# Kernel optimization log

Measured on AMD Instinct MI355X. Metric: run time of the kernel, lower is better.

The kernel has to match this reference:

```python
import jax, jax.numpy as jnp
import numpy as np

HID = 1024; INTER = 2048; NSTATE = 16; KCONV = 4; DTRANK = 64
NHEADS = 16; NKV = 4; HDIM = 64; VHDIM = 128; EPS = 1e-6
ATTN_H = HID; K_H = NKV * HDIM; V_H = NKV * VHDIM
LATENT = INTER + ATTN_H + K_H + V_H  # 3840


def rmsnorm(x, w, eps=EPS):
    return x * jax.lax.rsqrt(jnp.mean(x * x, axis=-1, keepdims=True) + eps) * w


def setup_inputs():
    key = jax.random.key(0)
    ks = jax.random.split(key, 8)
    B, S = 2, 2048
    s = 0.02
    x = jax.random.normal(ks[0], (B, S, HID), jnp.float32)
    W_in = jax.random.normal(ks[1], (LATENT + INTER, HID), jnp.float32) * s
    conv_w = jax.random.normal(ks[2], (INTER, KCONV), jnp.float32) * 0.2
    conv_b = jnp.zeros((INTER,), jnp.float32)
    W_x = jax.random.normal(ks[3], (DTRANK + 2 * NSTATE, INTER), jnp.float32) * s
    dt_ln_w = jnp.ones((DTRANK,), jnp.float32)
    B_ln_w = jnp.ones((NSTATE,), jnp.float32)
    C_ln_w = jnp.ones((NSTATE,), jnp.float32)
    W_dt = jax.random.normal(ks[4], (INTER, DTRANK), jnp.float32) * s
    b_dt = jnp.log(jnp.expm1(jnp.full((INTER,), 0.01, jnp.float32)))
    A_log = jnp.log(jnp.broadcast_to(jnp.arange(1, NSTATE + 1, dtype=jnp.float32)[None, :], (INTER, NSTATE)))
    D_param = jnp.ones((INTER,), jnp.float32)
    ln1_w = jnp.ones((INTER,), jnp.float32)
    ln2_w = jnp.ones((INTER,), jnp.float32)
    W_out = jax.random.normal(ks[5], (HID, INTER), jnp.float32) * s
    return {"x": x, "W_in": W_in, "conv_w": conv_w, "conv_b": conv_b, "W_x": W_x,
            "dt_ln_w": dt_ln_w, "B_ln_w": B_ln_w, "C_ln_w": C_ln_w, "W_dt": W_dt,
            "b_dt": b_dt, "A_log": A_log, "D_param": D_param, "ln1_w": ln1_w,
            "ln2_w": ln2_w, "W_out": W_out}


def reference(x, W_in, conv_w, conv_b, W_x, dt_ln_w, B_ln_w, C_ln_w, W_dt, b_dt,
              A_log, D_param, ln1_w, ln2_w, W_out):
    Bsz, S, _ = x.shape
    proj = x @ W_in.T  # [B,S,LATENT+INTER]
    q = proj[..., :ATTN_H]
    k = proj[..., ATTN_H:ATTN_H + K_H]
    v = proj[..., ATTN_H + K_H:ATTN_H + K_H + V_H]
    xs = proj[..., ATTN_H + K_H + V_H:LATENT]
    gate = proj[..., LATENT:]

    # depthwise causal conv1d + silu (causal_conv1d_fn)
    xt = xs.transpose(0, 2, 1)  # [B,D,S]
    xc = jax.lax.conv_general_dilated(xt, conv_w[:, None, :], (1,), [(KCONV - 1, 0)],
                                      feature_group_count=INTER,
                                      dimension_numbers=("NCH", "OIH", "NCH"))
    xc = jax.nn.silu(xc + conv_b[None, :, None]).transpose(0, 2, 1)  # [B,S,D]

    # input-dependent dt, B, C with inner RMSNorms
    ssm_p = xc @ W_x.T  # [B,S,DTRANK+2N]
    dt = rmsnorm(ssm_p[..., :DTRANK], dt_ln_w)
    Bm = rmsnorm(ssm_p[..., DTRANK:DTRANK + NSTATE], B_ln_w)
    Cm = rmsnorm(ssm_p[..., DTRANK + NSTATE:], C_ln_w)
    delta = jax.nn.softplus(dt @ W_dt.T + b_dt)  # [B,S,D] (delta_bias + softplus)
    A = -jnp.exp(A_log)  # [D,N]

    def step(h, inp):
        d_t, b_t, c_t, x_t = inp  # [B,D],[B,N],[B,N],[B,D]
        dA = jnp.exp(d_t[:, :, None] * A)  # [B,D,N]
        h = h * dA + (d_t * x_t)[:, :, None] * b_t[:, None, :]
        y = jnp.einsum("bdn,bn->bd", h, c_t)
        return h, y

    h0 = jnp.zeros((Bsz, INTER, NSTATE), x.dtype)
    _, ys = jax.lax.scan(step, h0, (delta.transpose(1, 0, 2), Bm.transpose(1, 0, 2),
                                    Cm.transpose(1, 0, 2), xc.transpose(1, 0, 2)))
    y = ys.transpose(1, 0, 2) + xc * D_param
    y = y * jax.nn.silu(gate)  # gated scan output [B,S,INTER]

    # causal GQA attention branch (no output proj; v_head_dim = INTER/NHEADS)
    qh = q.reshape(Bsz, S, NHEADS, HDIM).transpose(0, 2, 1, 3)
    kh = jnp.repeat(k.reshape(Bsz, S, NKV, HDIM), NHEADS // NKV, axis=2).transpose(0, 2, 1, 3)
    vh = jnp.repeat(v.reshape(Bsz, S, NKV, VHDIM), NHEADS // NKV, axis=2).transpose(0, 2, 1, 3)
    scores = jnp.einsum("bhqd,bhkd->bhqk", qh, kh) * (1.0 / float(np.sqrt(HDIM)))
    mask = jnp.tril(jnp.ones((S, S), bool))
    scores = jnp.where(mask, scores, jnp.finfo(scores.dtype).min)
    attn = jnp.einsum("bhqk,bhkd->bhqd", jax.nn.softmax(scores, axis=-1), vh)
    attn = attn.transpose(0, 2, 1, 3).reshape(Bsz, S, INTER)

    out = (rmsnorm(attn, ln1_w) + rmsnorm(y, ln2_w)) * 0.5
    return out @ W_out.T
```

## Files before the change

### kernel.cpp

```cpp
#include <hip/hip_runtime.h>
#include <stdint.h>

#define HID    1024
#define INTER  2048
#define NSTATE 16
#define DTRANK 64
#define NHEADS 16
#define NKV    4
#define HDIM   64
#define VHDIM  128
#define ATTN_H 1024
#define K_H    256
#define V_H    512
#define LATENT 3840
#define NCOLS  5888
#define BATCH  2
#define SEQ    2048
#define T_TOT  4096
#define NCHUNK 64
#define CHLEN  32
#define LOG2E  1.44269504f

typedef __bf16 bf16x8 __attribute__((ext_vector_type(8)));
typedef float  f32x4  __attribute__((ext_vector_type(4)));
typedef float  f32x4v __attribute__((ext_vector_type(4)));
typedef unsigned short u16x8 __attribute__((ext_vector_type(8)));

__device__ __forceinline__ float bf2f(unsigned short u) {
    return __uint_as_float(((unsigned int)u) << 16);
}
__device__ __forceinline__ unsigned short f2bf(float f) {
    unsigned int u = __float_as_uint(f);
    u = (u + 0x7fffu + ((u >> 16) & 1u)) >> 16;
    return (unsigned short)u;
}
__device__ __forceinline__ bf16x8 ldb8(const unsigned short* p) {
    return __builtin_bit_cast(bf16x8, *(const u16x8*)p);
}

typedef const __attribute__((address_space(1))) unsigned int* gas_ptr;
typedef __attribute__((address_space(3))) unsigned int* las_ptr;
__device__ __forceinline__ void load_lds16(const void* g, void* l) {
    __builtin_amdgcn_global_load_lds((gas_ptr)g, (las_ptr)l, 16, 0, 0);
}

__global__ void k_prep(const float* __restrict__ x, const float* __restrict__ W_in,
                       const float* __restrict__ W_dt, const float* __restrict__ W_out,
                       const float* __restrict__ W_x,
                       unsigned short* __restrict__ xbf, unsigned short* __restrict__ Winbf,
                       unsigned short* __restrict__ Wdtbf, unsigned short* __restrict__ Woutbf,
                       unsigned short* __restrict__ Wxpad) {
    int i = blockIdx.x * 256 + threadIdx.x;
    const float* src; unsigned short* dst; int off;
    if (i < 524288)        { src = x;     dst = xbf;    off = i; }
    else if (i < 1277952)  { src = W_in;  dst = Winbf;  off = i - 524288; }
    else if (i < 1294336)  { src = W_dt;  dst = Wdtbf;  off = i - 1277952; }
    else if (i < 1556480)  { src = W_out; dst = Woutbf; off = i - 1294336; }
    else {
        int e = (i - 1556480) * 8;
        int row = e >> 11, col = e & 2047;
        u16x8 o;
        if (row < DTRANK + 2 * NSTATE) {
#pragma unroll
            for (int k = 0; k < 8; k++) o[k] = f2bf(W_x[(size_t)row * INTER + col + k]);
        } else {
#pragma unroll
            for (int k = 0; k < 8; k++) o[k] = 0;
        }
        *(u16x8*)(Wxpad + e) = o;
        return;
    }
    f32x4v a = ((const f32x4v*)src)[2 * off];
    f32x4v b = ((const f32x4v*)src)[2 * off + 1];
    u16x8 o;
#pragma unroll
    for (int k = 0; k < 4; k++) { o[k] = f2bf(a[k]); o[k + 4] = f2bf(b[k]); }
    *(u16x8*)(dst + (size_t)off * 8) = o;
}

template <int NT>
__launch_bounds__(512)
__global__ void k_gemm8(const unsigned short* __restrict__ A, const unsigned short* __restrict__ B,
                        unsigned short* __restrict__ C, int lda, int ldb, int ldc) {
    __shared__ __align__(16) unsigned short As[3][256 * 64];
    __shared__ __align__(16) unsigned short Bs[3][128 * 64];
    const int tid = threadIdx.x;
    const int lane = tid & 63;
    const int w = tid >> 6;
    const int wm = w >> 1, wn = w & 1;
    const int l15 = lane & 15, hi = lane >> 4;
    const int nwg = gridDim.x * gridDim.y;
    int lin = blockIdx.y * gridDim.x + blockIdx.x;
    lin = (lin & 7) * (nwg >> 3) + (lin >> 3);
    const int bm = (lin / gridDim.x) * 256;
    const int bn = (lin % gridDim.x) * 128;

    const int srcCol = ((lane & 7) ^ (lane >> 3)) * 8;

    auto stageA = [&](int buf, int kt, int u) {
        int rsb = 64 * u + 8 * w;
        load_lds16(A + (size_t)(bm + rsb + (lane >> 3)) * lda + kt * 64 + srcCol, &As[buf][rsb * 64]);
    };
    auto stageB = [&](int buf, int kt, int u) {
        int rsb = 64 * u + 8 * w;
        load_lds16(B + (size_t)(bn + rsb + (lane >> 3)) * ldb + kt * 64 + srcCol, &Bs[buf][rsb * 64]);
    };

    f32x4 acc[4][4];
#pragma unroll
    for (int i = 0; i < 4; i++)
#pragma unroll
        for (int j = 0; j < 4; j++) acc[i][j] = (f32x4){0.f, 0.f, 0.f, 0.f};

    auto phase = [&](int buf, int kk, auto stageThunk, int vm) {
        bf16x8 a_[4], b_[4];
        const int cc = (kk << 2) + hi;
#pragma unroll
        for (int mi = 0; mi < 4; ++mi) {
            int row = 64 * wm + 16 * mi + l15;
            a_[mi] = ldb8(&As[buf][row * 64 + ((cc ^ (row & 7)) << 3)]);
        }
#pragma unroll
        for (int ni = 0; ni < 4; ++ni) {
            int row = 64 * wn + 16 * ni + l15;
            b_[ni] = ldb8(&Bs[buf][row * 64 + ((cc ^ (row & 7)) << 3)]);
        }
        stageThunk();
        if (vm == 1)      asm volatile("s_waitcnt vmcnt(6)" ::: "memory");
        else if (vm == 2) asm volatile("s_waitcnt vmcnt(0)" ::: "memory");
        __builtin_amdgcn_s_barrier();
        __builtin_amdgcn_s_setprio(1);
#pragma unroll
        for (int mi = 0; mi < 4; ++mi)
#pragma unroll
            for (int ni = 0; ni < 4; ++ni)
                acc[mi][ni] = __builtin_amdgcn_mfma_f32_16x16x32_bf16(a_[mi], b_[ni], acc[mi][ni], 0, 0, 0);
        __builtin_amdgcn_s_setprio(0);
        __builtin_amdgcn_s_barrier();
    };

#pragma unroll
    for (int u = 0; u < 4; ++u) stageA(0, 0, u);
    stageB(0, 0, 0); stageB(0, 0, 1);
#pragma unroll
    for (int u = 0; u < 4; ++u) stageA(1, 1, u);
    stageB(1, 1, 0); stageB(1, 1, 1);
    asm volatile("s_waitcnt vmcnt(6)" ::: "memory");
    __builtin_amdgcn_s_barrier();

    int buf = 0;
    for (int t = 0; t < NT; ++t) {
        const int kt = t + 2;
        const bool st = kt < NT;
        const int pbuf = (buf + 2 >= 3) ? buf - 1 : buf + 2;
        phase(buf, 0, [&] {
            if (st) { stageA(pbuf, kt, 0); stageA(pbuf, kt, 1); stageA(pbuf, kt, 2); }
        }, 0);
        phase(buf, 1, [&] {
            if (st) { stageA(pbuf, kt, 3); stageB(pbuf, kt, 0); stageB(pbuf, kt, 1); }
        }, st ? 1 : 2);
        buf = (buf + 1 >= 3) ? 0 : buf + 1;
    }

#pragma unroll
    for (int mi = 0; mi < 4; ++mi)
#pragma unroll
        for (int ni = 0; ni < 4; ++ni)
#pragma unroll
            for (int r = 0; r < 4; ++r) {
                int grow = bm + 64 * wm + 16 * mi + (hi << 2) + r;
                int gcol = bn + 64 * wn + 16 * ni + l15;
                C[(size_t)grow * ldc + gcol] = f2bf(acc[mi][ni][r]);
            }
}

template <int OUT_MODE>
__launch_bounds__(256)
__global__ void k_gemm(const unsigned short* __restrict__ A, const unsigned short* __restrict__ B,
                       void* __restrict__ Cout, const float* __restrict__ bias,
                       int M, int N, int K, int lda, int ldb, int ldc) {
    __shared__ __align__(16) unsigned short As[128 * 64];
    __shared__ __align__(16) unsigned short Bs[128 * 64];
    const int tid = threadIdx.x;
    const int lane = tid & 63;
    const int w = tid >> 6;
    const int wm = w >> 1, wn = w & 1;
    const int nwg = gridDim.x * gridDim.y;
    int lin = blockIdx.y * gridDim.x + blockIdx.x;
    lin = (lin & 7) * (nwg >> 3) + (lin >> 3);
    const int bm = (lin / gridDim.x) * 128, bn = (lin % gridDim.x) * 128;
    const size_t koff = (OUT_MODE == 3) ? (size_t)blockIdx.z * K : 0;

    f32x4 acc[4][4];
#pragma unroll
    for (int i = 0; i < 4; i++)
#pragma unroll
        for (int j = 0; j < 4; j++) acc[i][j] = (f32x4){0.f, 0.f, 0.f, 0.f};

    const int nk = K >> 6;
    for (int ks = 0; ks < nk; ++ks) {
        const int k0 = ks << 6;
#pragma unroll
        for (int i = 0; i < 4; ++i) {
            int qb = (w << 6) + (i << 8);
            int q = qb + lane;
            int row = q >> 3, c = q & 7;
            int csrc = c ^ (row & 7);
            load_lds16(A + (size_t)(bm + row) * lda + koff + k0 + csrc * 8, As + qb * 8);
            load_lds16(B + (size_t)(bn + row) * ldb + koff + k0 + csrc * 8, Bs + qb * 8);
        }
        __syncthreads();
#pragma unroll
        for (int kk = 0; kk < 2; ++kk) {
            bf16x8 af[4], bfr[4];
#pragma unroll
            for (int mi = 0; mi < 4; mi++) {
                int row = (wm << 6) + (mi << 4) + (lane & 15);
                int c = (kk << 2) + (lane >> 4);
                af[mi] = ldb8(As + row * 64 + (c ^ (row & 7)) * 8);
            }
#pragma unroll
            for (int ni = 0; ni < 4; ni++) {
                int row = (wn << 6) + (ni << 4) + (lane & 15);
                int c = (kk << 2) + (lane >> 4);
                bfr[ni] = ldb8(Bs + row * 64 + (c ^ (row & 7)) * 8);
            }
#pragma unroll
            for (int mi = 0; mi < 4; mi++)
#pragma unroll
                for (int ni = 0; ni < 4; ni++)
                    acc[mi][ni] = __builtin_amdgcn_mfma_f32_16x16x32_bf16(af[mi], bfr[ni], acc[mi][ni], 0, 0, 0);
        }
        __syncthreads();
    }
#pragma unroll
    for (int mi = 0; mi < 4; mi++)
#pragma unroll
        for (int ni = 0; ni < 4; ni++)
#pragma unroll
            for (int r = 0; r < 4; r++) {
                int grow = bm + (wm << 6) + (mi << 4) + ((lane >> 4) << 2) + r;
                int gcol = bn + (wn << 6) + (ni << 4) + (lane & 15);
                float v = acc[mi][ni][r];
                if (OUT_MODE == 0) {
                    ((unsigned short*)Cout)[(size_t)grow * ldc + gcol] = f2bf(v);
                } else if (OUT_MODE == 1) {
                    ((float*)Cout)[(size_t)grow * ldc + gcol] = v;
                } else if (OUT_MODE == 3) {
                    ((float*)Cout)[(size_t)blockIdx.z * M * ldc + (size_t)grow * ldc + gcol] = v;
                } else {
                    v += bias[gcol];
                    v = (v > 20.f) ? v : log1pf(__expf(v));
                    ((unsigned short*)Cout)[(size_t)grow * ldc + gcol] = f2bf(v);
                }
            }
}

__global__ void k_conv(const unsigned short* __restrict__ proj, const float* __restrict__ conv_w,
                       const float* __restrict__ conv_b, unsigned short* __restrict__ xc) {
    int r = blockIdx.x;
    int d8 = threadIdx.x * 8;
    int t = r & (SEQ - 1);
    float accv[8];
#pragma unroll
    for (int i = 0; i < 8; i++) accv[i] = conv_b[d8 + i];
#pragma unroll
    for (int j = 0; j < 4; j++) {
        int tp = t - 3 + j;
        if (tp < 0) continue;
        u16x8 xv = *(const u16x8*)(proj + (size_t)(r - 3 + j) * NCOLS + (LATENT - INTER) + d8);
#pragma unroll
        for (int i = 0; i < 8; i++) accv[i] += conv_w[(d8 + i) * 4 + j] * bf2f(xv[i]);
    }
    u16x8 o;
#pragma unroll
    for (int i = 0; i < 8; i++) {
        float v = accv[i];
        v = v / (1.f + __expf(-v));
        o[i] = f2bf(v);
    }
    *(u16x8*)(xc + (size_t)r * INTER + d8) = o;
}

__global__ void k_rms3(const float* __restrict__ ssmp, const float* __restrict__ dt_w,
                       const float* __restrict__ B_w, const float* __restrict__ C_w,
                       unsigned short* __restrict__ dtbf, float* __restrict__ Bm, float* __restrict__ Cm) {
    int r = blockIdx.x;
    int tid = threadIdx.x;
    int lane = tid & 63, w = tid >> 6;
    int c = tid;
    float v = 0.f;
    if (c < 96) {
#pragma unroll
        for (int s = 0; s < 8; s++) v += ssmp[(size_t)s * (T_TOT * 128) + (size_t)r * 128 + c];
    }
    float s = v * v;
    if (w == 0) {
#pragma unroll
        for (int d = 1; d < 64; d <<= 1) s += __shfl_xor(s, d);
        float rms = rsqrtf(s * (1.f / 64.f) + 1e-6f);
        dtbf[(size_t)r * 64 + lane] = f2bf(v * rms * dt_w[lane]);
    } else {
#pragma unroll
        for (int d = 1; d < 16; d <<= 1) s += __shfl_xor(s, d);
        float rms = rsqrtf(s * (1.f / 16.f) + 1e-6f);
        if (lane < 16) Bm[(size_t)r * 16 + lane] = v * rms * B_w[lane];
        else if (lane < 32) Cm[(size_t)r * 16 + (lane - 16)] = v * rms * C_w[lane - 16];
    }
}

template <int PASS>
__launch_bounds__(256)
__global__ void k_scan_chunk(const unsigned short* __restrict__ deltabf, const unsigned short* __restrict__ xcbf,
                             const float* __restrict__ Bm, const float* __restrict__ Cm,
                             const float* __restrict__ A_log,
                             float* __restrict__ hend, float* __restrict__ sumd,
                             const float* __restrict__ hinit, unsigned short* __restrict__ ybf) {
    __shared__ __align__(16) unsigned short dltS[CHLEN * 256];
    __shared__ __align__(16) unsigned short xvS[CHLEN * 256];
    __shared__ __align__(16) float BsT[CHLEN * 16];
    __shared__ __align__(16) float CsT[CHLEN * 16];
    const int d0 = blockIdx.x * 256;
    const int c = blockIdx.y;
    const int b = blockIdx.z;
    const int tid = threadIdx.x, lane = tid & 63, w = tid >> 6;
    const int t0 = c * CHLEN;
    const size_t rowbase = (size_t)(b * SEQ + t0);

    float An[16];
    {
        const f32x4* ap = (const f32x4*)(A_log + (size_t)(d0 + tid) * 16);
#pragma unroll
        for (int n4 = 0; n4 < 4; n4++) {
            f32x4 av = ap[n4];
#pragma unroll
            for (int j = 0; j < 4; j++) An[n4 * 4 + j] = -LOG2E * __expf(av[j]);
        }
    }

#pragma unroll
    for (int i = 0; i < 4; ++i) {
        int qb = (w << 6) + (i << 8);
        int q = qb + lane;
        int t = q >> 5, coff = q & 31;
        load_lds16(deltabf + (rowbase + t) * INTER + d0 + coff * 8, dltS + qb * 8);
        load_lds16(xcbf + (rowbase + t) * INTER + d0 + coff * 8, xvS + qb * 8);
    }
    if (tid < 128) {
        ((f32x4*)BsT)[tid] = ((const f32x4*)(Bm + rowbase * 16))[tid];
        if (PASS == 2) ((f32x4*)CsT)[tid] = ((const f32x4*)(Cm + rowbase * 16))[tid];
    }
    __syncthreads();

    const size_t sidx = ((size_t)(c * BATCH + b) * INTER + d0 + tid) * 16;
    float h[16];
    if (PASS == 2) {
        const f32x4* hp = (const f32x4*)(hinit + sidx);
#pragma unroll
        for (int n4 = 0; n4 < 4; n4++) {
            f32x4 hv = hp[n4];
#pragma unroll
            for (int j = 0; j < 4; j++) h[n4 * 4 + j] = hv[j];
        }
    } else {
#pragma unroll
        for (int n = 0; n < 16; n++) h[n] = 0.f;
    }
    float sd = 0.f;
    for (int t = 0; t < CHLEN; ++t) {
        float dlt = bf2f(dltS[t * 256 + tid]);
        float xv = bf2f(xvS[t * 256 + tid]);
        float dx = dlt * xv;
        if (PASS == 0) sd += dlt;
        float y = 0.f;
#pragma unroll
        for (int n4 = 0; n4 < 4; ++n4) {
            f32x4 Bt = ((f32x4*)BsT)[t * 4 + n4];
            f32x4 Ct;
            if (PASS == 2) Ct = ((f32x4*)CsT)[t * 4 + n4];
#pragma unroll
            for (int j = 0; j < 4; ++j) {
                int n = n4 * 4 + j;
                float a = exp2f(dlt * An[n]);
                h[n] = h[n] * a + dx * Bt[j];
                if (PASS == 2) y += h[n] * Ct[j];
            }
        }
        if (PASS == 2) ybf[(rowbase + t) * INTER + d0 + tid] = f2bf(y);
    }
    if (PASS == 0) {
        f32x4* hp = (f32x4*)(hend + sidx);
#pragma unroll
        for (int n4 = 0; n4 < 4; n4++) {
            f32x4 hv;
#pragma unroll
            for (int j = 0; j < 4; j++) hv[j] = h[n4 * 4 + j];
            hp[n4] = hv;
        }
        sumd[(size_t)(c * BATCH + b) * INTER + d0 + tid] = sd;
    }
}

__global__ void k_scan_prop(const float* __restrict__ A_log, const float* __restrict__ hend,
                            const float* __restrict__ sumd, float* __restrict__ hinit) {
    const int tid = blockIdx.x * 256 + threadIdx.x;
    const int n = tid & 15;
    const int d = (tid >> 4) & (INTER - 1);
    const float An = -LOG2E * __expf(A_log[(size_t)d * 16 + n]);
    const int bd = tid >> 4;
    float h = 0.f;
#pragma unroll 1
    for (int cb = 0; cb < NCHUNK / 4; ++cb) {
        float he[4], sdv[4];
#pragma unroll
        for (int j = 0; j < 4; j++) {
            int c = cb * 4 + j;
            he[j] = hend[(size_t)c * 65536 + tid];
            sdv[j] = sumd[(size_t)c * 4096 + bd];
        }
#pragma unroll
        for (int j = 0; j < 4; j++) {
            int c = cb * 4 + j;
            hinit[(size_t)c * 65536 + tid] = h;
            h = he[j] + exp2f(An * sdv[j]) * h;
        }
    }
}

__launch_bounds__(256)
__global__ void k_attn(const unsigned short* __restrict__ proj, unsigned short* __restrict__ attn) {
    __shared__ __align__(16) unsigned short Ks[64 * 64];
    __shared__ __align__(16) unsigned short Vt[128 * 64];
    __shared__ __align__(16) unsigned short Ps[4 * 16 * 64];
    const int pair = blockIdx.x;
    const int h = blockIdx.y;
    const int b = blockIdx.z;
    const int g = h >> 2;
    const int tid = threadIdx.x, lane = tid & 63, w = tid >> 6;
    const int l15 = lane & 15, hi = lane >> 4;

    const int krow = tid >> 3, kc = tid & 7;
    const int kp2 = (tid & 31) * 2, vb = tid >> 5;

    const unsigned short* kbase = proj + (size_t)(b * SEQ) * NCOLS + ATTN_H + g * HDIM;
    const unsigned short* vbase = proj + (size_t)(b * SEQ) * NCOLS + (ATTN_H + K_H) + g * VHDIM;

    u16x8 krA[2], vrA[2][2], krB[2], vrB[2][2];

    auto LOAD = [&](u16x8* kr, u16x8 (*vr)[2], int kv) {
        const unsigned short* kp_ = kbase + (size_t)(kv + krow) * NCOLS + kc * 8;
        kr[0] = *(const u16x8*)kp_;
        kr[1] = *(const u16x8*)(kp_ + (size_t)32 * NCOLS);
        const unsigned short* vp_ = vbase + (size_t)(kv + kp2) * NCOLS + vb * 8;
        vr[0][0] = *(const u16x8*)vp_;
        vr[0][1] = *(const u16x8*)(vp_ + NCOLS);
        vr[1][0] = *(const u16x8*)(vp_ + 64);
        vr[1][1] = *(const u16x8*)(vp_ + NCOLS + 64);
    };
    auto WRITE = [&](u16x8* kr, u16x8 (*vr)[2]) {
        int ksw = (kc ^ (krow & 7)) << 3;
        *(u16x8*)&Ks[krow * 64 + ksw] = kr[0];
        *(u16x8*)&Ks[(krow + 32) * 64 + ksw] = kr[1];
#pragma unroll
        for (int hf = 0; hf < 2; hf++) {
            u16x8 va = vr[hf][0], vb2 = vr[hf][1];
#pragma unroll
            for (int i = 0; i < 8; i++) {
                unsigned int pk = (unsigned int)va[i] | ((unsigned int)vb2[i] << 16);
                int r = (vb + hf * 8) * 8 + i;
                *(unsigned int*)&Vt[r * 64 + (((kp2 >> 3) ^ (r & 7)) << 3) + (kp2 & 7)] = pk;
            }
        }
    };

    const float SC = 0.18033688f;

    for (int phase = 0; phase < 2; ++phase) {
        const int qt = (phase == 0) ? (31 - pair) : pair;
        const int qw = qt * 64 + w * 16;
        const int ntiles = qt + 1;

        bf16x8 qf[2];
        {
            int qr = qw + l15;
            const unsigned short* qp = proj + (size_t)(b * SEQ + qr) * NCOLS + h * HDIM + hi * 8;
            qf[0] = ldb8(qp);
            qf[1] = ldb8(qp + 32);
        }
        f32x4 O[8];
#pragma unroll
        for (int vf = 0; vf < 8; vf++) O[vf] = (f32x4){0.f, 0.f, 0.f, 0.f};
        float l_[4] = {0.f, 0.f, 0.f, 0.f};

        auto COMPUTE = [&](int kv, bool MASK) {
            const int pbase = w * 1024;
            f32x4 sv[4];
#pragma unroll
            for (int cf = 0; cf < 4; ++cf) {
                f32x4 s = (f32x4){0.f, 0.f, 0.f, 0.f};
                int row = cf * 16 + l15;
#pragma unroll
                for (int kk = 0; kk < 2; ++kk) {
                    bf16x8 kb = ldb8(&Ks[row * 64 + ((((kk << 2) + hi) ^ (row & 7)) << 3)]);
                    s = __builtin_amdgcn_mfma_f32_16x16x32_bf16(qf[kk], kb, s, 0, 0, 0);
                }
                sv[cf] = s;
            }
            const int qi0 = qw + (hi << 2);
#pragma unroll
            for (int cf = 0; cf < 4; ++cf) {
                int ki = kv + cf * 16 + l15;
#pragma unroll
                for (int rg = 0; rg < 4; ++rg) {
                    float v;
                    if (MASK) v = (ki <= qi0 + rg) ? exp2f(sv[cf][rg] * SC) : 0.f;
                    else      v = exp2f(sv[cf][rg] * SC);
                    l_[rg] += v;
                    int pr = (hi << 2) + rg;
                    int pc = cf * 16 + l15;
                    Ps[pbase + pr * 64 + (((pc >> 3) ^ (pr & 7)) << 3) + (pc & 7)] = f2bf(v);
                }
            }
            bf16x8 pa0 = ldb8(&Ps[pbase + l15 * 64 + ((hi ^ (l15 & 7)) << 3)]);
            bf16x8 pa1 = ldb8(&Ps[pbase + l15 * 64 + (((4 + hi) ^ (l15 & 7)) << 3)]);
#pragma unroll
            for (int vf = 0; vf < 8; ++vf) {
                int vr_ = vf * 16 + l15;
                bf16x8 v0 = ldb8(&Vt[vr_ * 64 + ((hi ^ (vr_ & 7)) << 3)]);
                bf16x8 v1 = ldb8(&Vt[vr_ * 64 + (((4 + hi) ^ (vr_ & 7)) << 3)]);
                O[vf] = __builtin_amdgcn_mfma_f32_16x16x32_bf16(pa0, v0, O[vf], 0, 0, 0);
                O[vf] = __builtin_amdgcn_mfma_f32_16x16x32_bf16(pa1, v1, O[vf], 0, 0, 0);
            }
        };

        LOAD(krA, vrA, 0);
        bool useA = true;
        for (int j = 0; j < ntiles; ++j) {
            if (useA) {
                WRITE(krA, vrA);
                if (j + 1 < ntiles) LOAD(krB, vrB, (j + 1) * 64);
            } else {
                WRITE(krB, vrB);
                if (j + 1 < ntiles) LOAD(krA, vrA, (j + 1) * 64);
            }
            __syncthreads();
            COMPUTE(j * 64, j == ntiles - 1);
            __syncthreads();
            useA = !useA;
        }

#pragma unroll
        for (int dd = 1; dd < 16; dd <<= 1)
#pragma unroll
            for (int rg = 0; rg < 4; ++rg) l_[rg] += __shfl_xor(l_[rg], dd);
#pragma unroll
        for (int rg = 0; rg < 4; ++rg) {
            float inv = 1.f / l_[rg];
            int grow = b * SEQ + qw + (hi << 2) + rg;
#pragma unroll
            for (int vf = 0; vf < 8; ++vf) {
                int gcol = h * VHDIM + vf * 16 + l15;
                attn[(size_t)grow * INTER + gcol] = f2bf(O[vf][rg] * inv);
            }
        }
    }
}

__launch_bounds__(256)
__global__ void k_fuse(const unsigned short* __restrict__ attn, const unsigned short* __restrict__ ybf,
                       const unsigned short* __restrict__ xc, const unsigned short* __restrict__ proj,
                       const float* __restrict__ Dp, const float* __restrict__ ln1,
                       const float* __restrict__ ln2, unsigned short* __restrict__ fused) {
    __shared__ float red[8];
    int r = blockIdx.x, tid = threadIdx.x;
    int c8 = tid * 8;
    u16x8 av = *(const u16x8*)(attn + (size_t)r * INTER + c8);
    u16x8 yv8 = *(const u16x8*)(ybf + (size_t)r * INTER + c8);
    u16x8 xv8 = *(const u16x8*)(xc + (size_t)r * INTER + c8);
    u16x8 gv8 = *(const u16x8*)(proj + (size_t)r * NCOLS + LATENT + c8);
    float a_[8], y_[8];
    float ssa = 0.f, ssy = 0.f;
#pragma unroll
    for (int i = 0; i < 8; i++) {
        float a = bf2f(av[i]);
        float yv = bf2f(yv8[i]) + bf2f(xv8[i]) * Dp[c8 + i];
        float gg = bf2f(gv8[i]);
        yv *= gg / (1.f + __expf(-gg));
        a_[i] = a; y_[i] = yv;
        ssa += a * a; ssy += yv * yv;
    }
#pragma unroll
    for (int d = 1; d < 64; d <<= 1) { ssa += __shfl_xor(ssa, d); ssy += __shfl_xor(ssy, d); }
    int w = tid >> 6, lane = tid & 63;
    if (lane == 0) { red[w * 2] = ssa; red[w * 2 + 1] = ssy; }
    __syncthreads();
    ssa = red[0] + red[2] + red[4] + red[6];
    ssy = red[1] + red[3] + red[5] + red[7];
    float ra = rsqrtf(ssa * (1.f / 2048.f) + 1e-6f);
    float ry = rsqrtf(ssy * (1.f / 2048.f) + 1e-6f);
    u16x8 o;
#pragma unroll
    for (int i = 0; i < 8; i++) {
        float v = (a_[i] * ra * ln1[c8 + i] + y_[i] * ry * ln2[c8 + i]) * 0.5f;
        o[i] = f2bf(v);
    }
    *(u16x8*)(fused + (size_t)r * INTER + c8) = o;
}

extern "C" void kernel_launch(void* const* d_in, const int* in_sizes, int n_in,
                              void* d_out, int out_size, void* d_ws, size_t ws_size,
                              hipStream_t stream) {
    const float* x      = (const float*)d_in[0];
    const float* W_in   = (const float*)d_in[1];
    const float* conv_w = (const float*)d_in[2];
    const float* conv_b = (const float*)d_in[3];
    const float* W_x    = (const float*)d_in[4];
    const float* dt_w   = (const float*)d_in[5];
    const float* B_w    = (const float*)d_in[6];
    const float* C_w    = (const float*)d_in[7];
    const float* W_dt   = (const float*)d_in[8];
    const float* b_dt   = (const float*)d_in[9];
    const float* A_log  = (const float*)d_in[10];
    const float* Dp     = (const float*)d_in[11];
    const float* ln1    = (const float*)d_in[12];
    const float* ln2    = (const float*)d_in[13];
    const float* W_out  = (const float*)d_in[14];
    float* out = (float*)d_out;

    char* p = (char*)d_ws;
    auto alloc = [&](size_t bytes) -> void* {
        void* r = (void*)p;
        p += (bytes + 255) & ~(size_t)255;
        return r;
    };
    unsigned short* xbf     = (unsigned short*)alloc((size_t)T_TOT * HID * 2);
    unsigned short* Winbf   = (unsigned short*)alloc((size_t)NCOLS * HID * 2);
    unsigned short* projbf  = (unsigned short*)alloc((size_t)T_TOT * NCOLS * 2);
    unsigned short* xcbf    = (unsigned short*)alloc((size_t)T_TOT * INTER * 2);
    unsigned short* Wxpad   = (unsigned short*)alloc((size_t)128 * INTER * 2);
    float*          ssmp    = (float*)alloc((size_t)8 * T_TOT * 128 * 4);
    unsigned short* dtbf    = (unsigned short*)alloc((size_t)T_TOT * DTRANK * 2);
    float*          Bm      = (float*)alloc((size_t)T_TOT * 16 * 4);
    float*          Cm      = (float*)alloc((size_t)T_TOT * 16 * 4);
    unsigned short* Wdtbf   = (unsigned short*)alloc((size_t)INTER * DTRANK * 2);
    unsigned short* deltabf = (unsigned short*)alloc((size_t)T_TOT * INTER * 2);
    unsigned short* ybf     = (unsigned short*)alloc((size_t)T_TOT * INTER * 2);
    unsigned short* attnbf  = (unsigned short*)alloc((size_t)T_TOT * INTER * 2);
    unsigned short* fusedbf = (unsigned short*)alloc((size_t)T_TOT * INTER * 2);
    unsigned short* Woutbf  = (unsigned short*)alloc((size_t)HID * INTER * 2);
    float*          hendws  = (float*)alloc((size_t)NCHUNK * BATCH * INTER * 16 * 4);
    float*          hinitws = (float*)alloc((size_t)NCHUNK * BATCH * INTER * 16 * 4);
    float*          sumdws  = (float*)alloc((size_t)NCHUNK * BATCH * INTER * 4);

    k_prep<<<6208, 256, 0, stream>>>(x, W_in, W_dt, W_out, W_x, xbf, Winbf, Wdtbf, Woutbf, Wxpad);

    k_gemm8<16><<<dim3(NCOLS / 128, T_TOT / 256), 512, 0, stream>>>(
        xbf, Winbf, projbf, HID, HID, NCOLS);
    k_conv<<<T_TOT, 256, 0, stream>>>(projbf, conv_w, conv_b, xcbf);
    k_gemm<3><<<dim3(1, T_TOT / 128, 8), 256, 0, stream>>>(
        xcbf, Wxpad, ssmp, nullptr, T_TOT, 128, 256, INTER, INTER, 128);
    k_rms3<<<T_TOT, 128, 0, stream>>>(ssmp, dt_w, B_w, C_w, dtbf, Bm, Cm);
    k_gemm<2><<<dim3(INTER / 128, T_TOT / 128), 256, 0, stream>>>(
        dtbf, Wdtbf, deltabf, b_dt, T_TOT, INTER, DTRANK, DTRANK, DTRANK, INTER);
    k_scan_chunk<0><<<dim3(INTER / 256, NCHUNK, BATCH), 256, 0, stream>>>(
        deltabf, xcbf, Bm, Cm, A_log, hendws, sumdws, nullptr, nullptr);
    k_scan_prop<<<256, 256, 0, stream>>>(A_log, hendws, sumdws, hinitws);
    k_scan_chunk<2><<<dim3(INTER / 256, NCHUNK, BATCH), 256, 0, stream>>>(
        deltabf, xcbf, Bm, Cm, A_log, nullptr, nullptr, hinitws, ybf);
    k_attn<<<dim3(16, NHEADS, BATCH), 256, 0, stream>>>(projbf, attnbf);
    k_fuse<<<T_TOT, 256, 0, stream>>>(attnbf, ybf, xcbf, projbf, Dp, ln1, ln2, fusedbf);
    k_gemm<1><<<dim3(HID / 128, T_TOT / 128), 256, 0, stream>>>(
        fusedbf, Woutbf, out, nullptr, T_TOT, HID, INTER, INTER, INTER, HID);
}
```

Before: 407.8 us.

## Keep attention probabilities in registers, double-buffer K/V in LDS, split-K output GEMM

The attention kernel swaps the MFMA operand order so scores come out transposed. The probability matrix is then packed to bf16 with v_cvt_pk and rearranged with lane shuffles, replacing the LDS round-trip through the Ps buffer. K/V tiles now use two LDS buffers, with the next tile loaded during compute, so each iteration needs one barrier instead of two. Separately, the output projection GEMM is split along K into two partial fp32 results that a new elementwise kernel adds, raising block count at the cost of extra memory traffic and one more launch.

Result: no change. 413.7 us (+1.5%).

```diff
diff --git a/kernel.cpp b/kernel.cpp
--- a/kernel.cpp
+++ b/kernel.cpp
@@ -25,6 +25,7 @@
 typedef float  f32x4  __attribute__((ext_vector_type(4)));
 typedef float  f32x4v __attribute__((ext_vector_type(4)));
 typedef unsigned short u16x8 __attribute__((ext_vector_type(8)));
+typedef unsigned int   u32x4 __attribute__((ext_vector_type(4)));
 
 __device__ __forceinline__ float bf2f(unsigned short u) {
     return __uint_as_float(((unsigned int)u) << 16);
@@ -36,6 +37,11 @@
 }
 __device__ __forceinline__ bf16x8 ldb8(const unsigned short* p) {
     return __builtin_bit_cast(bf16x8, *(const u16x8*)p);
+}
+__device__ __forceinline__ unsigned int cvtpk(float lo, float hi_) {
+    unsigned int r;
+    asm("v_cvt_pk_bf16_f32 %0, %1, %2" : "=v"(r) : "v"(lo), "v"(hi_));
+    return r;
 }
 
 typedef const __attribute__((address_space(1))) unsigned int* gas_ptr;
@@ -256,6 +262,13 @@
             }
 }
 
+__global__ void k_addout(const float* __restrict__ part, float* __restrict__ out) {
+    int i = blockIdx.x * 256 + threadIdx.x;
+    f32x4 a = ((const f32x4*)part)[i];
+    f32x4 b = ((const f32x4*)(part + (size_t)T_TOT * HID))[i];
+    ((f32x4*)out)[i] = a + b;
+}
+
 __global__ void k_conv(const unsigned short* __restrict__ proj, const float* __restrict__ conv_w,
                        const float* __restrict__ conv_b, unsigned short* __restrict__ xc) {
     int r = blockIdx.x;
@@ -429,9 +442,8 @@
 
 __launch_bounds__(256)
 __global__ void k_attn(const unsigned short* __restrict__ proj, unsigned short* __restrict__ attn) {
-    __shared__ __align__(16) unsigned short Ks[64 * 64];
-    __shared__ __align__(16) unsigned short Vt[128 * 64];
-    __shared__ __align__(16) unsigned short Ps[4 * 16 * 64];
+    __shared__ __align__(16) unsigned short Ks[2][64 * 64];
+    __shared__ __align__(16) unsigned short Vt[2][128 * 64];
     const int pair = blockIdx.x;
     const int h = blockIdx.y;
     const int b = blockIdx.z;
@@ -445,9 +457,9 @@
     const unsigned short* kbase = proj + (size_t)(b * SEQ) * NCOLS + ATTN_H + g * HDIM;
     const unsigned short* vbase = proj + (size_t)(b * SEQ) * NCOLS + (ATTN_H + K_H) + g * VHDIM;
 
-    u16x8 krA[2], vrA[2][2], krB[2], vrB[2][2];
-
-    auto LOAD = [&](u16x8* kr, u16x8 (*vr)[2], int kv) {
+    u16x8 kr[2], vr[2][2];
+
+    auto LOAD = [&](int kv) {
         const unsigned short* kp_ = kbase + (size_t)(kv + krow) * NCOLS + kc * 8;
         kr[0] = *(const u16x8*)kp_;
         kr[1] = *(const u16x8*)(kp_ + (size_t)32 * NCOLS);
@@ -457,10 +469,10 @@
         vr[1][0] = *(const u16x8*)(vp_ + 64);
         vr[1][1] = *(const u16x8*)(vp_ + NCOLS + 64);
     };
-    auto WRITE = [&](u16x8* kr, u16x8 (*vr)[2]) {
+    auto WRITE = [&](int nb) {
         int ksw = (kc ^ (krow & 7)) << 3;
-        *(u16x8*)&Ks[krow * 64 + ksw] = kr[0];
-        *(u16x8*)&Ks[(krow + 32) * 64 + ksw] = kr[1];
+        *(u16x8*)&Ks[nb][krow * 64 + ksw] = kr[0];
+        *(u16x8*)&Ks[nb][(krow + 32) * 64 + ksw] = kr[1];
 #pragma unroll
         for (int hf = 0; hf < 2; hf++) {
             u16x8 va = vr[hf][0], vb2 = vr[hf][1];
@@ -468,17 +480,21 @@
             for (int i = 0; i < 8; i++) {
                 unsigned int pk = (unsigned int)va[i] | ((unsigned int)vb2[i] << 16);
                 int r = (vb + hf * 8) * 8 + i;
-                *(unsigned int*)&Vt[r * 64 + (((kp2 >> 3) ^ (r & 7)) << 3) + (kp2 & 7)] = pk;
+                *(unsigned int*)&Vt[nb][r * 64 + (((kp2 >> 3) ^ (r & 7)) << 3) + (kp2 & 7)] = pk;
             }
         }
     };
 
     const float SC = 0.18033688f;
+    const int srcA = ((hi & 1) << 5) + l15;
+    const int srcB = srcA + 16;
+    const bool cfs = (hi >> 1) != 0;
 
     for (int phase = 0; phase < 2; ++phase) {
         const int qt = (phase == 0) ? (31 - pair) : pair;
         const int qw = qt * 64 + w * 16;
         const int ntiles = qt + 1;
+        const int qi = qw + l15;
 
         bf16x8 qf[2];
         {
@@ -490,10 +506,9 @@
         f32x4 O[8];
 #pragma unroll
         for (int vf = 0; vf < 8; vf++) O[vf] = (f32x4){0.f, 0.f, 0.f, 0.f};
-        float l_[4] = {0.f, 0.f, 0.f, 0.f};
-
-        auto COMPUTE = [&](int kv, bool MASK) {
-            const int pbase = w * 1024;
+        float l_ = 0.f;
+
+        auto COMPUTE = [&](int kv, bool MASK, int cb) {
             f32x4 sv[4];
 #pragma unroll
             for (int cf = 0; cf < 4; ++cf) {
@@ -501,66 +516,73 @@
                 int row = cf * 16 + l15;
 #pragma unroll
                 for (int kk = 0; kk < 2; ++kk) {
-                    bf16x8 kb = ldb8(&Ks[row * 64 + ((((kk << 2) + hi) ^ (row & 7)) << 3)]);
-                    s = __builtin_amdgcn_mfma_f32_16x16x32_bf16(qf[kk], kb, s, 0, 0, 0);
+                    bf16x8 kb = ldb8(&Ks[cb][row * 64 + ((((kk << 2) + hi) ^ (row & 7)) << 3)]);
+                    s = __builtin_amdgcn_mfma_f32_16x16x32_bf16(kb, qf[kk], s, 0, 0, 0);
                 }
                 sv[cf] = s;
             }
-            const int qi0 = qw + (hi << 2);
+            unsigned int wv[4][2];
 #pragma unroll
             for (int cf = 0; cf < 4; ++cf) {
-                int ki = kv + cf * 16 + l15;
+                int kb0 = kv + cf * 16 + (hi << 2);
+                float vv[4];
 #pragma unroll
                 for (int rg = 0; rg < 4; ++rg) {
-                    float v;
-                    if (MASK) v = (ki <= qi0 + rg) ? exp2f(sv[cf][rg] * SC) : 0.f;
-                    else      v = exp2f(sv[cf][rg] * SC);
-                    l_[rg] += v;
-                    int pr = (hi << 2) + rg;
-                    int pc = cf * 16 + l15;
-                    Ps[pbase + pr * 64 + (((pc >> 3) ^ (pr & 7)) << 3) + (pc & 7)] = f2bf(v);
+                    float e = exp2f(sv[cf][rg] * SC);
+                    vv[rg] = (MASK && (kb0 + rg > qi)) ? 0.f : e;
                 }
-            }
-            bf16x8 pa0 = ldb8(&Ps[pbase + l15 * 64 + ((hi ^ (l15 & 7)) << 3)]);
-            bf16x8 pa1 = ldb8(&Ps[pbase + l15 * 64 + (((4 + hi) ^ (l15 & 7)) << 3)]);
-#pragma unroll
-            for (int vf = 0; vf < 8; ++vf) {
-                int vr_ = vf * 16 + l15;
-                bf16x8 v0 = ldb8(&Vt[vr_ * 64 + ((hi ^ (vr_ & 7)) << 3)]);
-                bf16x8 v1 = ldb8(&Vt[vr_ * 64 + (((4 + hi) ^ (vr_ & 7)) << 3)]);
-                O[vf] = __builtin_amdgcn_mfma_f32_16x16x32_bf16(pa0, v0, O[vf], 0, 0, 0);
-                O[vf] = __builtin_amdgcn_mfma_f32_16x16x32_bf16(pa1, v1, O[vf], 0, 0, 0);
+                l_ += (vv[0] + vv[1]) + (vv[2] + vv[3]);
+                wv[cf][0] = cvtpk(vv[0], vv[1]);
+                wv[cf][1] = cvtpk(vv[2], vv[3]);
+            }
+#pragma unroll
+            for (int kk2 = 0; kk2 < 2; ++kk2) {
+                unsigned int p00 = wv[2 * kk2][0],     p01 = wv[2 * kk2][1];
+                unsigned int p10 = wv[2 * kk2 + 1][0], p11 = wv[2 * kk2 + 1][1];
+                unsigned int sA00 = (unsigned int)__shfl((int)p00, srcA);
+                unsigned int sA01 = (unsigned int)__shfl((int)p01, srcA);
+                unsigned int sB00 = (unsigned int)__shfl((int)p00, srcB);
+                unsigned int sB01 = (unsigned int)__shfl((int)p01, srcB);
+                unsigned int sA10 = (unsigned int)__shfl((int)p10, srcA);
+                unsigned int sA11 = (unsigned int)__shfl((int)p11, srcA);
+                unsigned int sB10 = (unsigned int)__shfl((int)p10, srcB);
+                unsigned int sB11 = (unsigned int)__shfl((int)p11, srcB);
+                u32x4 fw;
+                fw[0] = cfs ? sA10 : sA00;
+                fw[1] = cfs ? sA11 : sA01;
+                fw[2] = cfs ? sB10 : sB00;
+                fw[3] = cfs ? sB11 : sB01;
+                bf16x8 pa = __builtin_bit_cast(bf16x8, fw);
+#pragma unroll
+                for (int vf = 0; vf < 8; ++vf) {
+                    int vr_ = vf * 16 + l15;
+                    bf16x8 vv2 = ldb8(&Vt[cb][vr_ * 64 + ((((kk2 << 2) + hi) ^ (vr_ & 7)) << 3)]);
+                    O[vf] = __builtin_amdgcn_mfma_f32_16x16x32_bf16(pa, vv2, O[vf], 0, 0, 0);
+                }
             }
         };
 
-        LOAD(krA, vrA, 0);
-        bool useA = true;
+        LOAD(0);
+        WRITE(0);
+        __syncthreads();
         for (int j = 0; j < ntiles; ++j) {
-            if (useA) {
-                WRITE(krA, vrA);
-                if (j + 1 < ntiles) LOAD(krB, vrB, (j + 1) * 64);
-            } else {
-                WRITE(krB, vrB);
-                if (j + 1 < ntiles) LOAD(krA, vrA, (j + 1) * 64);
-            }
+            if (j + 1 < ntiles) LOAD((j + 1) * 64);
+            COMPUTE(j * 64, j == ntiles - 1, j & 1);
+            if (j + 1 < ntiles) WRITE((j + 1) & 1);
             __syncthreads();
-            COMPUTE(j * 64, j == ntiles - 1);
-            __syncthreads();
-            useA = !useA;
-        }
-
-#pragma unroll
-        for (int dd = 1; dd < 16; dd <<= 1)
-#pragma unroll
-            for (int rg = 0; rg < 4; ++rg) l_[rg] += __shfl_xor(l_[rg], dd);
+        }
+
+        l_ += __shfl_xor(l_, 16);
+        l_ += __shfl_xor(l_, 32);
+        float inv = 1.f / l_;
 #pragma unroll
         for (int rg = 0; rg < 4; ++rg) {
-            float inv = 1.f / l_[rg];
+            float linv = __shfl(inv, (hi << 2) + rg);
             int grow = b * SEQ + qw + (hi << 2) + rg;
 #pragma unroll
             for (int vf = 0; vf < 8; ++vf) {
                 int gcol = h * VHDIM + vf * 16 + l15;
-                attn[(size_t)grow * INTER + gcol] = f2bf(O[vf][rg] * inv);
+                attn[(size_t)grow * INTER + gcol] = f2bf(O[vf][rg] * linv);
             }
         }
     }
@@ -651,6 +673,7 @@
     float*          hendws  = (float*)alloc((size_t)NCHUNK * BATCH * INTER * 16 * 4);
     float*          hinitws = (float*)alloc((size_t)NCHUNK * BATCH * INTER * 16 * 4);
     float*          sumdws  = (float*)alloc((size_t)NCHUNK * BATCH * INTER * 4);
+    float*          outpart = (float*)alloc((size_t)2 * T_TOT * HID * 4);
 
     k_prep<<<6208, 256, 0, stream>>>(x, W_in, W_dt, W_out, W_x, xbf, Winbf, Wdtbf, Woutbf, Wxpad);
 
@@ -669,6 +692,7 @@
         deltabf, xcbf, Bm, Cm, A_log, nullptr, nullptr, hinitws, ybf);
     k_attn<<<dim3(16, NHEADS, BATCH), 256, 0, stream>>>(projbf, attnbf);
     k_fuse<<<T_TOT, 256, 0, stream>>>(attnbf, ybf, xcbf, projbf, Dp, ln1, ln2, fusedbf);
-    k_gemm<1><<<dim3(HID / 128, T_TOT / 128), 256, 0, stream>>>(
-        fusedbf, Woutbf, out, nullptr, T_TOT, HID, INTER, INTER, INTER, HID);
-}
+    k_gemm<3><<<dim3(HID / 128, T_TOT / 128, 2), 256, 0, stream>>>(
+        fusedbf, Woutbf, outpart, nullptr, T_TOT, HID, 1024, INTER, INTER, HID);
+    k_addout<<<T_TOT * HID / 1024, 256, 0, stream>>>(outpart, out);
+}
```
